# Kernel tuning notes

Hardware: AMD Instinct MI355X
Metric: run time of the kernel (lower is better)

The kernel has to match this reference:

```python
import jax, jax.numpy as jnp
import numpy as np

FFT_SIZE = 2046
MSE_WEIGHT = 0.7
DELAY_WEIGHT = 0.3
ENERGY_EPS = 1e-8
RANGE_EPS = 1e-8
TEMP_SCALE = 10.0


def setup_inputs() -> dict:
    key = jax.random.key(0)
    k1, k2 = jax.random.split(key)
    shape = (32, 64, 4, 1024)  # [batch, bs_ant, ue_ant, subcarriers]
    predicted_csi = jax.random.normal(k1, shape, dtype=jnp.float32)
    target_csi = jax.random.normal(k2, shape, dtype=jnp.float32)
    return {"predicted_csi": predicted_csi, "target_csi": target_csi}


def _compute_pdp(csi):
    # Real input is treated as complex with zero imaginary part (as in torch module).
    n = csi.shape[-1]
    if n < FFT_SIZE:
        pad = [(0, 0)] * (csi.ndim - 1) + [(0, FFT_SIZE - n)]
        csi = jnp.pad(csi, pad)
    else:
        csi = csi[..., :FFT_SIZE]
    td = jnp.fft.ifft(csi.astype(jnp.complex64), axis=-1)  # [..., FFT_SIZE]
    return jnp.abs(td) ** 2


def _normalize_pdp(pdp):
    # Per-sample (last-axis) energy normalization; skip if energy ~ 0.
    energy = jnp.sum(pdp, axis=-1, keepdims=True)
    return jnp.where(energy < ENERGY_EPS, pdp, pdp / energy)


def _soft_delay(pdp):
    # Adaptive-temperature soft-argmax delay per sample.
    f = pdp.shape[-1]
    idx = jnp.arange(f, dtype=jnp.float32)
    rng = jnp.clip(jnp.max(pdp, -1, keepdims=True) - jnp.min(pdp, -1, keepdims=True), RANGE_EPS)
    weights = jax.nn.softmax(pdp * (TEMP_SCALE / rng), axis=-1)
    return jnp.sum(idx * weights, axis=-1)


def reference(predicted_csi, target_csi):
    pdp_pred = _normalize_pdp(_compute_pdp(predicted_csi))  # [B, BS, UE, FFT_SIZE]
    pdp_tgt = _normalize_pdp(_compute_pdp(target_csi))
    # MSE per sample is mean over FFT_SIZE; averaging over samples/antenna pairs == global mean.
    mse_loss = jnp.mean((pdp_pred - pdp_tgt) ** 2)
    delay_diff = jnp.abs(_soft_delay(pdp_pred) - _soft_delay(pdp_tgt)) / FFT_SIZE
    delay_loss = jnp.mean(delay_diff)
    return MSE_WEIGHT * mse_loss + DELAY_WEIGHT * delay_loss
```

## Files before the change

kernel.cpp:

```cpp
#include <hip/hip_runtime.h>
#include <math.h>

#define IN_N   1024
#define NROWS  8192
#define NTOT   16384
#define FFT_N  2046

typedef unsigned short u16;
typedef __attribute__((ext_vector_type(8))) __bf16 bf16x8;
typedef __attribute__((ext_vector_type(4))) float  f32x4;

__device__ __forceinline__ u16 f2bf(float f) {
    unsigned u = __builtin_bit_cast(unsigned, f);
    unsigned r = (u + 0x7fffu + ((u >> 16) & 1u)) >> 16;
    return (u16)r;
}
__device__ __forceinline__ float bf2f(u16 h) {
    unsigned u = ((unsigned)h) << 16;
    return __builtin_bit_cast(float, u);
}

__device__ __forceinline__ void gload_lds16(const void* g, void* l) {
    __builtin_amdgcn_global_load_lds(
        (__attribute__((address_space(1))) void*)g,
        (__attribute__((address_space(3))) void*)l, 16, 0, 0);
}

__global__ __launch_bounds__(256) void prep_kernel(
    const float* __restrict__ pred, const float* __restrict__ tgt,
    u16* __restrict__ Wc, u16* __restrict__ Ws, u16* __restrict__ Xh) {
    int bid = blockIdx.x;
    if (bid < 1024) {
        int k = bid;
        int n0 = threadIdx.x * 4;
        const float c = 6.28318530717958647692f / 2046.0f;
        ushort4 oc, os;
        #pragma unroll
        for (int i = 0; i < 4; ++i) {
            int n = n0 + i;
            int m = (k * n) % FFT_N;
            float a = (float)m * c;
            float sv, cv;
            __sincosf(a, &sv, &cv);
            ((u16*)&oc)[i] = f2bf(cv);
            ((u16*)&os)[i] = f2bf(sv);
        }
        size_t o = (size_t)k * IN_N + n0;
        *(ushort4*)(Wc + o) = oc;
        *(ushort4*)(Ws + o) = os;
    } else {
        size_t gid = (size_t)(bid - 1024) * 256 + threadIdx.x;
        size_t e = gid * 4;
        const size_t half = (size_t)NROWS * IN_N;
        const float* s = (e < half) ? (pred + e) : (tgt + (e - half));
        float4 v = *(const float4*)s;
        ushort4 o;
        o.x = f2bf(v.x); o.y = f2bf(v.y); o.z = f2bf(v.z); o.w = f2bf(v.w);
        *(ushort4*)(Xh + e) = o;
    }
}

#define BM 128
#define BN 256
#define BK 32
#define NKT 32

#define FENCE() asm volatile("" ::: "memory")

__global__ __launch_bounds__(512, 2) void dft_pdp_mfma(
    const u16* __restrict__ Wc, const u16* __restrict__ Ws,
    const u16* __restrict__ Xh, u16* __restrict__ pdp) {

    __shared__ __align__(16) char lds[4][32768];

    const int bid  = blockIdx.x;
    const int xcd  = bid & 7;
    const int slot = bid >> 3;
    const int m0 = (slot & 7) * BM;
    const int r0 = (xcd * 8 + (slot >> 3)) * BN;

    const int t    = threadIdx.x;
    const int w    = t >> 6;
    const int lane = t & 63;
    const int wm = (w & 1) * 64;
    const int wr = (w >> 1) * 64;
    const int lr = lane & 15;
    const int rdoff = (((lane >> 4) ^ ((lane >> 1) & 3)) << 4);

    const int srow  = t >> 2;
    const int sslot = (t & 3) ^ ((t >> 3) & 3);
    const size_t aOfs  = (size_t)(m0 + srow) * 2048 + sslot * 16;
    const size_t xOfs0 = (size_t)(r0 + srow) * 2048 + sslot * 16;
    const size_t xOfs1 = (size_t)(r0 + 128 + srow) * 2048 + sslot * 16;
    const int woff = w << 10;

    f32x4 accRe[4][4], accIm[4][4];
    #pragma unroll
    for (int i = 0; i < 4; ++i)
        #pragma unroll
        for (int j = 0; j < 4; ++j)
            #pragma unroll
            for (int q = 0; q < 4; ++q) { accRe[i][j][q] = 0.f; accIm[i][j][q] = 0.f; }

    #define STAGE(buf, kt) do { \
        gload_lds16((const char*)Wc + aOfs + (size_t)(kt) * 64, &lds[buf][0] + woff); \
        gload_lds16((const char*)Ws + aOfs + (size_t)(kt) * 64, &lds[buf][0] + 8192 + woff); \
        gload_lds16((const char*)Xh + xOfs0 + (size_t)(kt) * 64, &lds[buf][0] + 16384 + woff); \
        gload_lds16((const char*)Xh + xOfs1 + (size_t)(kt) * 64, &lds[buf][0] + 24576 + woff); \
    } while (0)
    #define LDA(buf, off)  (*(const bf16x8*)(&lds[buf][0] + (wm + (off) + lr) * 64 + rdoff))
    #define LDSN(buf, off) (*(const bf16x8*)(&lds[buf][0] + 8192 + (wm + (off) + lr) * 64 + rdoff))
    #define LDX(buf, j)    (*(const bf16x8*)(&lds[buf][0] + 16384 + (wr + (j) * 16 + lr) * 64 + rdoff))

    bf16x8 fa0, fa1, fa2, fa3, fs0, fs1, fs2, fs3;
    bf16x8 fbE0, fbE1, fbE2, fbE3, fbO0, fbO1, fbO2, fbO3;

    #define CLUSTER(i, FA, FS, B0, B1, B2, B3) do { \
        accRe[i][0] = __builtin_amdgcn_mfma_f32_16x16x32_bf16(FA, B0, accRe[i][0], 0, 0, 0); \
        accIm[i][0] = __builtin_amdgcn_mfma_f32_16x16x32_bf16(FS, B0, accIm[i][0], 0, 0, 0); \
        accRe[i][1] = __builtin_amdgcn_mfma_f32_16x16x32_bf16(FA, B1, accRe[i][1], 0, 0, 0); \
        accIm[i][1] = __builtin_amdgcn_mfma_f32_16x16x32_bf16(FS, B1, accIm[i][1], 0, 0, 0); \
        accRe[i][2] = __builtin_amdgcn_mfma_f32_16x16x32_bf16(FA, B2, accRe[i][2], 0, 0, 0); \
        accIm[i][2] = __builtin_amdgcn_mfma_f32_16x16x32_bf16(FS, B2, accIm[i][2], 0, 0, 0); \
        accRe[i][3] = __builtin_amdgcn_mfma_f32_16x16x32_bf16(FA, B3, accRe[i][3], 0, 0, 0); \
        accIm[i][3] = __builtin_amdgcn_mfma_f32_16x16x32_bf16(FS, B3, accIm[i][3], 0, 0, 0); \
    } while (0)

    #define TILE(kt, C0, C1, C2, C3, N0, N1, N2, N3) do { \
        const int bn_ = ((kt) + 1) & 3; \
         \
        if ((kt) <= NKT - 3) asm volatile("s_waitcnt vmcnt(4)" ::: "memory"); \
        else                 asm volatile("s_waitcnt vmcnt(0)" ::: "memory"); \
        __builtin_amdgcn_s_barrier(); \
        FENCE(); \
        if ((kt) + 1 < NKT) {             \
            N0 = LDX(bn_, 0); N1 = LDX(bn_, 1); N2 = LDX(bn_, 2); N3 = LDX(bn_, 3); \
        } \
        if ((kt) + 3 < NKT) STAGE(((kt) + 3) & 3, (kt) + 3); \
        if ((kt) + 1 < NKT) asm volatile("s_waitcnt lgkmcnt(4)" ::: "memory"); \
        else                asm volatile("s_waitcnt lgkmcnt(0)" ::: "memory"); \
        __builtin_amdgcn_sched_barrier(0); \
        __builtin_amdgcn_s_setprio(1); \
        CLUSTER(0, fa0, fs0, C0, C1, C2, C3); \
        if ((kt) + 1 < NKT) { fa0 = LDA(bn_, 0);  fs0 = LDSN(bn_, 0);  } \
        CLUSTER(1, fa1, fs1, C0, C1, C2, C3); \
        if ((kt) + 1 < NKT) { fa1 = LDA(bn_, 16); fs1 = LDSN(bn_, 16); } \
        CLUSTER(2, fa2, fs2, C0, C1, C2, C3); \
        if ((kt) + 1 < NKT) { fa2 = LDA(bn_, 32); fs2 = LDSN(bn_, 32); } \
        CLUSTER(3, fa3, fs3, C0, C1, C2, C3); \
        if ((kt) + 1 < NKT) { fa3 = LDA(bn_, 48); fs3 = LDSN(bn_, 48); } \
        __builtin_amdgcn_s_setprio(0); \
    } while (0)

    STAGE(0, 0); STAGE(1, 1); STAGE(2, 2);
    asm volatile("s_waitcnt vmcnt(8)" ::: "memory");
    __builtin_amdgcn_s_barrier();
    FENCE();
    fbE0 = LDX(0, 0); fbE1 = LDX(0, 1); fbE2 = LDX(0, 2); fbE3 = LDX(0, 3);
    fa0 = LDA(0, 0);  fa1 = LDA(0, 16); fa2 = LDA(0, 32); fa3 = LDA(0, 48);
    fs0 = LDSN(0, 0); fs1 = LDSN(0, 16); fs2 = LDSN(0, 32); fs3 = LDSN(0, 48);

    for (int kt2 = 0; kt2 < NKT; kt2 += 2) {
        TILE(kt2,     fbE0, fbE1, fbE2, fbE3, fbO0, fbO1, fbO2, fbO3);
        TILE(kt2 + 1, fbO0, fbO1, fbO2, fbO3, fbE0, fbE1, fbE2, fbE3);
    }
    #undef TILE
    #undef CLUSTER
    #undef STAGE
    #undef LDA
    #undef LDSN
    #undef LDX

    const float inv = 1.0f / ((float)FFT_N * (float)FFT_N);
    #pragma unroll
    for (int i = 0; i < 4; ++i)
        #pragma unroll
        for (int j = 0; j < 4; ++j) {
            int m = m0 + wm + i * 16 + (lane >> 4) * 4;
            int r = r0 + wr + j * 16 + (lane & 15);
            ushort4 o;
            #pragma unroll
            for (int q = 0; q < 4; ++q) {
                float re = accRe[i][j][q], im = accIm[i][j][q];
                ((u16*)&o)[q] = f2bf((re * re + im * im) * inv);
            }
            *(ushort4*)(pdp + (size_t)r * IN_N + m) = o;
        }
}

__device__ __forceinline__ float wsum(float v) {
    #pragma unroll
    for (int m = 32; m >= 1; m >>= 1) v += __shfl_xor(v, m);
    return v;
}
__device__ __forceinline__ float wmax(float v) {
    #pragma unroll
    for (int m = 32; m >= 1; m >>= 1) v = fmaxf(v, __shfl_xor(v, m));
    return v;
}
__device__ __forceinline__ float wmin(float v) {
    #pragma unroll
    for (int m = 32; m >= 1; m >>= 1) v = fminf(v, __shfl_xor(v, m));
    return v;
}

__global__ __launch_bounds__(256) void row_stats_kernel(
    const u16* __restrict__ pdp,
    float* __restrict__ mse_rows, float* __restrict__ dd_rows) {

    const int wid  = threadIdx.x >> 6;
    const int lane = threadIdx.x & 63;
    const int r = blockIdx.x * 4 + wid;
    const u16* pp = pdp + (size_t)r * IN_N + lane * 16;
    const u16* pt = pdp + (size_t)(NROWS + r) * IN_N + lane * 16;

    uint4 v0 = *(const uint4*)pp;       uint4 v1 = *(const uint4*)(pp + 8);
    uint4 u0 = *(const uint4*)pt;       uint4 u1 = *(const uint4*)(pt + 8);
    float a[16], b[16];
    {
        unsigned pw[8] = {v0.x, v0.y, v0.z, v0.w, v1.x, v1.y, v1.z, v1.w};
        unsigned tw[8] = {u0.x, u0.y, u0.z, u0.w, u1.x, u1.y, u1.z, u1.w};
        #pragma unroll
        for (int i = 0; i < 8; ++i) {
            a[2*i]   = bf2f((u16)(pw[i] & 0xffffu));
            a[2*i+1] = bf2f((u16)(pw[i] >> 16));
            b[2*i]   = bf2f((u16)(tw[i] & 0xffffu));
            b[2*i+1] = bf2f((u16)(tw[i] >> 16));
        }
    }

    float wsp = 0.f, wst = 0.f;
    float mxp = -1e30f, mnp = 1e30f, mxt = -1e30f, mnt = 1e30f;
    #pragma unroll
    for (int i = 0; i < 16; ++i) {
        int k = lane * 16 + i;
        float wgt = (k == 0 || k == 1023) ? 1.f : 2.f;
        wsp += wgt * a[i];        wst += wgt * b[i];
        mxp = fmaxf(mxp, a[i]);   mnp = fminf(mnp, a[i]);
        mxt = fmaxf(mxt, b[i]);   mnt = fminf(mnt, b[i]);
    }
    float Ep  = wsum(wsp);
    float Et  = wsum(wst);
    float Mp  = wmax(mxp);
    float mp_ = wmin(mnp);
    float Mt  = wmax(mxt);
    float mt_ = wmin(mnt);

    float scp = (Ep < 1e-8f) ? 1.f : 1.f / Ep;
    float sct = (Et < 1e-8f) ? 1.f : 1.f / Et;
    float rngp = fmaxf(scp * (Mp - mp_), 1e-8f);
    float rngt = fmaxf(sct * (Mt - mt_), 1e-8f);
    float cfp = 10.f * scp / rngp;
    float cft = 10.f * sct / rngt;
    float smp = cfp * Mp;
    float smt = cft * Mt;

    float zp = 0.f, zt = 0.f, ms = 0.f;
    #pragma unroll
    for (int i = 0; i < 16; ++i) {
        int k = lane * 16 + i;
        float wgt = (k == 0 || k == 1023) ? 1.f : 2.f;
        zp += wgt * __expf(cfp * a[i] - smp);
        zt += wgt * __expf(cft * b[i] - smt);
        float d = a[i] * scp - b[i] * sct;
        ms += wgt * d * d;
    }
    float Zp  = wsum(zp);
    float Zt  = wsum(zt);
    float MSE = wsum(ms);

    if (lane == 0) {
        float w0p = __expf(cfp * a[0] - smp) / Zp;
        float w0t = __expf(cft * b[0] - smt) / Zt;
        mse_rows[r] = MSE;
        dd_rows[r]  = 0.5f * fabsf(w0p - w0t);
    }
}

__global__ __launch_bounds__(256) void final_kernel(
    const float* __restrict__ mse_rows, const float* __restrict__ dd_rows,
    float* __restrict__ out) {
    __shared__ float r1[256];
    __shared__ float r2[256];
    int t = threadIdx.x;
    float s1 = 0.f, s2 = 0.f;
    for (int r = t; r < NROWS; r += 256) { s1 += mse_rows[r]; s2 += dd_rows[r]; }
    r1[t] = s1; r2[t] = s2;
    __syncthreads();
    for (int s = 128; s > 0; s >>= 1) {
        if (t < s) { r1[t] += r1[t + s]; r2[t] += r2[t + s]; }
        __syncthreads();
    }
    if (t == 0) {
        float mse = r1[0] / ((float)NROWS * (float)FFT_N);
        float dl  = r2[0] / (float)NROWS;
        out[0] = 0.7f * mse + 0.3f * dl;
    }
}

extern "C" void kernel_launch(void* const* d_in, const int* in_sizes, int n_in,
                              void* d_out, int out_size, void* d_ws, size_t ws_size,
                              hipStream_t stream) {
    const float* pred = (const float*)d_in[0];
    const float* tgt  = (const float*)d_in[1];
    float* out = (float*)d_out;

    char* ws = (char*)d_ws;
    u16* Xh   = (u16*)ws;
    u16* Wch  = (u16*)(ws + (size_t)32 * 1024 * 1024);
    u16* Wsh  = (u16*)(ws + (size_t)34 * 1024 * 1024);
    u16* pdp  = (u16*)(ws + (size_t)40 * 1024 * 1024);
    float* mse_rows = (float*)(ws + (size_t)72 * 1024 * 1024);
    float* dd_rows  = mse_rows + NROWS;

    prep_kernel<<<1024 + NTOT * IN_N / 4 / 256, 256, 0, stream>>>(pred, tgt, Wch, Wsh, Xh);

    dft_pdp_mfma<<<512, 512, 0, stream>>>(Wch, Wsh, Xh, pdp);

    row_stats_kernel<<<NROWS / 4, 256, 0, stream>>>(pdp, mse_rows, dd_rows);
    final_kernel<<<1, 256, 0, stream>>>(mse_rows, dd_rows, out);
}
```

Measured before the change: 111.1 us.

## Fuse fp32-to-bf16 input conversion into DFT GEMM loads

Removes the separate input conversion pass that wrote a bf16 copy of the inputs, and the prep kernel now only builds twiddle tables. The GEMM kernel loads fp32 inputs straight into registers, packs them to bf16, and writes them to swizzled LDS with a restructured pipeline, since async global-to-LDS loads cannot convert. This saves a full read/write pass over the inputs, but the GEMM now reads twice as many X bytes, uses more registers, and waits on vmcnt(0) every tile, which may expose load latency.

```diff
diff --git a/kernel.cpp b/kernel.cpp
--- a/kernel.cpp
+++ b/kernel.cpp
@@ -15,6 +15,9 @@
     unsigned r = (u + 0x7fffu + ((u >> 16) & 1u)) >> 16;
     return (u16)r;
 }
+__device__ __forceinline__ unsigned pk2(float a, float b) {
+    return (unsigned)f2bf(a) | ((unsigned)f2bf(b) << 16);
+}
 __device__ __forceinline__ float bf2f(u16 h) {
     unsigned u = ((unsigned)h) << 16;
     return __builtin_bit_cast(float, u);
@@ -26,38 +29,24 @@
         (__attribute__((address_space(3))) void*)l, 16, 0, 0);
 }
 
-__global__ __launch_bounds__(256) void prep_kernel(
-    const float* __restrict__ pred, const float* __restrict__ tgt,
-    u16* __restrict__ Wc, u16* __restrict__ Ws, u16* __restrict__ Xh) {
-    int bid = blockIdx.x;
-    if (bid < 1024) {
-        int k = bid;
-        int n0 = threadIdx.x * 4;
-        const float c = 6.28318530717958647692f / 2046.0f;
-        ushort4 oc, os;
-        #pragma unroll
-        for (int i = 0; i < 4; ++i) {
-            int n = n0 + i;
-            int m = (k * n) % FFT_N;
-            float a = (float)m * c;
-            float sv, cv;
-            __sincosf(a, &sv, &cv);
-            ((u16*)&oc)[i] = f2bf(cv);
-            ((u16*)&os)[i] = f2bf(sv);
-        }
-        size_t o = (size_t)k * IN_N + n0;
-        *(ushort4*)(Wc + o) = oc;
-        *(ushort4*)(Ws + o) = os;
-    } else {
-        size_t gid = (size_t)(bid - 1024) * 256 + threadIdx.x;
-        size_t e = gid * 4;
-        const size_t half = (size_t)NROWS * IN_N;
-        const float* s = (e < half) ? (pred + e) : (tgt + (e - half));
-        float4 v = *(const float4*)s;
-        ushort4 o;
-        o.x = f2bf(v.x); o.y = f2bf(v.y); o.z = f2bf(v.z); o.w = f2bf(v.w);
-        *(ushort4*)(Xh + e) = o;
-    }
+__global__ void twiddle_kernel(u16* __restrict__ Wc, u16* __restrict__ Ws) {
+    int k = blockIdx.x;
+    int n0 = threadIdx.x * 4;
+    const float c = 6.28318530717958647692f / 2046.0f;
+    ushort4 oc, os;
+    #pragma unroll
+    for (int i = 0; i < 4; ++i) {
+        int n = n0 + i;
+        int m = (k * n) % FFT_N;
+        float a = (float)m * c;
+        float sv, cv;
+        __sincosf(a, &sv, &cv);
+        ((u16*)&oc)[i] = f2bf(cv);
+        ((u16*)&os)[i] = f2bf(sv);
+    }
+    size_t o = (size_t)k * IN_N + n0;
+    *(ushort4*)(Wc + o) = oc;
+    *(ushort4*)(Ws + o) = os;
 }
 
 #define BM 128
@@ -68,8 +57,9 @@
 #define FENCE() asm volatile("" ::: "memory")
 
 __global__ __launch_bounds__(512, 2) void dft_pdp_mfma(
+    const float* __restrict__ pred, const float* __restrict__ tgt,
     const u16* __restrict__ Wc, const u16* __restrict__ Ws,
-    const u16* __restrict__ Xh, u16* __restrict__ pdp) {
+    u16* __restrict__ pdp) {
 
     __shared__ __align__(16) char lds[4][32768];
 
@@ -89,10 +79,17 @@
 
     const int srow  = t >> 2;
     const int sslot = (t & 3) ^ ((t >> 3) & 3);
-    const size_t aOfs  = (size_t)(m0 + srow) * 2048 + sslot * 16;
-    const size_t xOfs0 = (size_t)(r0 + srow) * 2048 + sslot * 16;
-    const size_t xOfs1 = (size_t)(r0 + 128 + srow) * 2048 + sslot * 16;
+    const size_t aOfs = (size_t)(m0 + srow) * 2048 + sslot * 16;
     const int woff = w << 10;
+
+    const float* xsrc = (r0 < NROWS) ? (pred + (size_t)r0 * IN_N)
+                                     : (tgt + (size_t)(r0 - NROWS) * IN_N);
+    const int xrow = t >> 1;
+    const int xc0  = (t & 1) * 2;
+    const int xsw  = (xrow >> 1) & 3;
+    const float* xbase = xsrc + (size_t)xrow * IN_N + (t & 1) * 16;
+    const int xwo0 = 16384 + xrow * 64 + (((xc0    ) ^ xsw) << 4);
+    const int xwo1 = 16384 + xrow * 64 + (((xc0 | 1) ^ xsw) << 4);
 
     f32x4 accRe[4][4], accIm[4][4];
     #pragma unroll
@@ -102,12 +99,22 @@
             #pragma unroll
             for (int q = 0; q < 4; ++q) { accRe[i][j][q] = 0.f; accIm[i][j][q] = 0.f; }
 
-    #define STAGE(buf, kt) do { \
+    float4 xq0, xq1, xq2, xq3;
+
+    #define XL(kt) do { const float* p_ = xbase + (size_t)(kt) * 32; \
+        xq0 = *(const float4*)(p_);      xq1 = *(const float4*)(p_ + 4); \
+        xq2 = *(const float4*)(p_ + 8);  xq3 = *(const float4*)(p_ + 12); } while (0)
+    #define XWRITE(buf) do { \
+        uint4 a_, b_; \
+        a_.x = pk2(xq0.x, xq0.y); a_.y = pk2(xq0.z, xq0.w); \
+        a_.z = pk2(xq1.x, xq1.y); a_.w = pk2(xq1.z, xq1.w); \
+        b_.x = pk2(xq2.x, xq2.y); b_.y = pk2(xq2.z, xq2.w); \
+        b_.z = pk2(xq3.x, xq3.y); b_.w = pk2(xq3.z, xq3.w); \
+        *(uint4*)(&lds[buf][0] + xwo0) = a_; \
+        *(uint4*)(&lds[buf][0] + xwo1) = b_; } while (0)
+    #define STAGE_AS(buf, kt) do { \
         gload_lds16((const char*)Wc + aOfs + (size_t)(kt) * 64, &lds[buf][0] + woff); \
-        gload_lds16((const char*)Ws + aOfs + (size_t)(kt) * 64, &lds[buf][0] + 8192 + woff); \
-        gload_lds16((const char*)Xh + xOfs0 + (size_t)(kt) * 64, &lds[buf][0] + 16384 + woff); \
-        gload_lds16((const char*)Xh + xOfs1 + (size_t)(kt) * 64, &lds[buf][0] + 24576 + woff); \
-    } while (0)
+        gload_lds16((const char*)Ws + aOfs + (size_t)(kt) * 64, &lds[buf][0] + 8192 + woff); } while (0)
     #define LDA(buf, off)  (*(const bf16x8*)(&lds[buf][0] + (wm + (off) + lr) * 64 + rdoff))
     #define LDSN(buf, off) (*(const bf16x8*)(&lds[buf][0] + 8192 + (wm + (off) + lr) * 64 + rdoff))
     #define LDX(buf, j)    (*(const bf16x8*)(&lds[buf][0] + 16384 + (wr + (j) * 16 + lr) * 64 + rdoff))
@@ -128,15 +135,16 @@
 
     #define TILE(kt, C0, C1, C2, C3, N0, N1, N2, N3) do { \
         const int bn_ = ((kt) + 1) & 3; \
-         \
-        if ((kt) <= NKT - 3) asm volatile("s_waitcnt vmcnt(4)" ::: "memory"); \
-        else                 asm volatile("s_waitcnt vmcnt(0)" ::: "memory"); \
+        const int bx_ = ((kt) + 2) & 3; \
+        asm volatile("s_waitcnt vmcnt(0)" ::: "memory"); \
         __builtin_amdgcn_s_barrier(); \
         FENCE(); \
-        if ((kt) + 1 < NKT) {             \
+        if ((kt) + 2 < NKT) XWRITE(bx_);           \
+        if ((kt) + 1 < NKT) {                      \
             N0 = LDX(bn_, 0); N1 = LDX(bn_, 1); N2 = LDX(bn_, 2); N3 = LDX(bn_, 3); \
         } \
-        if ((kt) + 3 < NKT) STAGE(((kt) + 3) & 3, (kt) + 3); \
+        if ((kt) + 2 < NKT) STAGE_AS(bx_, (kt) + 2); \
+        if ((kt) + 3 < NKT) XL((kt) + 3); \
         if ((kt) + 1 < NKT) asm volatile("s_waitcnt lgkmcnt(4)" ::: "memory"); \
         else                asm volatile("s_waitcnt lgkmcnt(0)" ::: "memory"); \
         __builtin_amdgcn_sched_barrier(0); \
@@ -152,8 +160,15 @@
         __builtin_amdgcn_s_setprio(0); \
     } while (0)
 
-    STAGE(0, 0); STAGE(1, 1); STAGE(2, 2);
-    asm volatile("s_waitcnt vmcnt(8)" ::: "memory");
+    XL(0);
+    STAGE_AS(0, 0); STAGE_AS(1, 1);
+    asm volatile("s_waitcnt vmcnt(0)" ::: "memory");
+    XWRITE(0);
+    XL(1);
+    asm volatile("s_waitcnt vmcnt(0)" ::: "memory");
+    XWRITE(1);
+    XL(2);
+    asm volatile("s_waitcnt lgkmcnt(0)" ::: "memory");
     __builtin_amdgcn_s_barrier();
     FENCE();
     fbE0 = LDX(0, 0); fbE1 = LDX(0, 1); fbE2 = LDX(0, 2); fbE3 = LDX(0, 3);
@@ -166,7 +181,9 @@
     }
     #undef TILE
     #undef CLUSTER
-    #undef STAGE
+    #undef STAGE_AS
+    #undef XL
+    #undef XWRITE
     #undef LDA
     #undef LDSN
     #undef LDX
@@ -306,16 +323,15 @@
     float* out = (float*)d_out;
 
     char* ws = (char*)d_ws;
-    u16* Xh   = (u16*)ws;
-    u16* Wch  = (u16*)(ws + (size_t)32 * 1024 * 1024);
-    u16* Wsh  = (u16*)(ws + (size_t)34 * 1024 * 1024);
-    u16* pdp  = (u16*)(ws + (size_t)40 * 1024 * 1024);
-    float* mse_rows = (float*)(ws + (size_t)72 * 1024 * 1024);
+    u16* Wch  = (u16*)ws;
+    u16* Wsh  = (u16*)(ws + (size_t)2 * 1024 * 1024);
+    u16* pdp  = (u16*)(ws + (size_t)4 * 1024 * 1024);
+    float* mse_rows = (float*)(ws + (size_t)40 * 1024 * 1024);
     float* dd_rows  = mse_rows + NROWS;
 
-    prep_kernel<<<1024 + NTOT * IN_N / 4 / 256, 256, 0, stream>>>(pred, tgt, Wch, Wsh, Xh);
-
-    dft_pdp_mfma<<<512, 512, 0, stream>>>(Wch, Wsh, Xh, pdp);
+    twiddle_kernel<<<1024, 256, 0, stream>>>(Wch, Wsh);
+
+    dft_pdp_mfma<<<512, 512, 0, stream>>>(pred, tgt, Wch, Wsh, pdp);
 
     row_stats_kernel<<<NROWS / 4, 256, 0, stream>>>(pdp, mse_rows, dd_rows);
     final_kernel<<<1, 256, 0, stream>>>(mse_rows, dd_rows, out);
```

After: 115.6 us. +4.0%, slower.
